# Kernel tuning notes

Measured on AMD Instinct MI355X. Metric: run time of the kernel, lower is better.

## Reference

```python
import jax, jax.numpy as jnp
import numpy as np

H = 64        # hidden_size
G = 64        # global_hidden_size
VOCAB = 128   # VOCAB_SIZE
NUM_OPS = 20
DEPTH = 12    # complete binary tree: 2**DEPTH - 1 nodes
B = 128       # batch of trees
TEMP = 3.0    # self.temperature


def setup_inputs() -> dict:
    key = jax.random.key(0)
    ks = jax.random.split(key, 16)
    s = 0.05
    N = 2 ** DEPTH - 1
    inp = {
        "x_idx": jax.random.randint(ks[0], (B, N), 0, VOCAB, dtype=jnp.int32),
        "validity_mask": jnp.ones((NUM_OPS,), jnp.float32),
        # binary tree-LSTM (blstm): x one-hot -> gates [i, f_a, f_b, o, u]
        "Wx": jax.random.normal(ks[1], (VOCAB, 5 * H), jnp.float32) * s,
        "Ua": jax.random.normal(ks[2], (H, 5 * H), jnp.float32) * s,
        "Ub": jax.random.normal(ks[3], (H, 5 * H), jnp.float32) * s,
        "b_tree": jnp.zeros((5 * H,), jnp.float32),
        # global nn.LSTM (1 layer), gate order i,f,g,o
        "W_ih": jax.random.normal(ks[4], (H, 4 * G), jnp.float32) * s,
        "W_hh": jax.random.normal(ks[5], (G, 4 * G), jnp.float32) * s,
        "b_lstm": jnp.zeros((4 * G,), jnp.float32),
        # FFN on root hidden
        "W1": jax.random.normal(ks[6], (H, H), jnp.float32) * s,
        "b1": jnp.zeros((H,), jnp.float32),
        "W2": jax.random.normal(ks[7], (H, H), jnp.float32) * s,
        "b2": jnp.zeros((H,), jnp.float32),
        # actor head on [hidden ; global_hidden]
        "actor_W": jax.random.normal(ks[8], (H + G, NUM_OPS), jnp.float32) * s,
        "actor_b": jnp.zeros((NUM_OPS,), jnp.float32),
    }
    return inp


def _tree_lstm_sweep(x_idx, Wx, Ua, Ub, b_tree):
    """Bottom-up binary tree-LSTM over a complete binary tree.
    Node i's children sit at flat positions 2i+1, 2i+2 (level layout)."""
    h_prev = c_prev = None
    for d in range(DEPTH - 1, -1, -1):
        n = 2 ** d
        off = n - 1
        # memory-bound gather of gate pre-activations: [B, n, 5H]
        z = Wx[x_idx[:, off:off + n]] + b_tree
        if h_prev is not None:
            h_a, h_b = h_prev[:, 0::2], h_prev[:, 1::2]
            c_a, c_b = c_prev[:, 0::2], c_prev[:, 1::2]
            z = z + jnp.einsum("bnh,hg->bng", h_a, Ua) + jnp.einsum("bnh,hg->bng", h_b, Ub)
        i, fa, fb, o, u = jnp.split(z, 5, axis=-1)
        c = jax.nn.sigmoid(i) * jnp.tanh(u)
        if h_prev is not None:
            c = c + jax.nn.sigmoid(fa) * c_a + jax.nn.sigmoid(fb) * c_b
        h = jax.nn.sigmoid(o) * jnp.tanh(c)
        h_prev, c_prev = h, c
    return h_prev[:, 0]  # root hidden [B, H]


def reference(x_idx, validity_mask, Wx, Ua, Ub, b_tree, W_ih, W_hh, b_lstm,
              W1, b1, W2, b2, actor_W, actor_b):
    h_root = _tree_lstm_sweep(x_idx, Wx, Ua, Ub, b_tree)
    # internal op 1: apply_ffn then apply_global_lstm
    f = jnp.maximum(h_root @ W1 + b1, 0.0) @ W2 + b2          # FFN [B, H]
    h0 = jnp.zeros((f.shape[0], G), f.dtype)
    g = f @ W_ih + h0 @ W_hh + b_lstm                          # one LSTM step
    i, fg, gg, o = jnp.split(g, 4, axis=-1)                    # torch order i,f,g,o
    c_g = jax.nn.sigmoid(i) * jnp.tanh(gg)                     # c0 = 0
    h_g = jax.nn.sigmoid(o) * jnp.tanh(c_g)                    # [B, G]
    # external actor with validity-masked weights (as in policy())
    feats = jnp.concatenate([f, h_g], axis=-1)                 # [B, H+G]
    logits = jnp.log(validity_mask) + feats @ (actor_W * validity_mask) + actor_b * validity_mask
    return jax.nn.softmax(logits / TEMP, axis=-1)              # [B, NUM_OPS]
```

## Files before the change

kernel.cpp:

```cpp
#include <hip/hip_runtime.h>


typedef unsigned short u16;
typedef unsigned int   u32;
typedef __attribute__((ext_vector_type(8))) short  short8;
typedef __attribute__((ext_vector_type(4))) float  floatx4;

#define L2E  1.44269504f
#define L2E2 2.885390082f

__device__ __forceinline__ float frcp(float x) { return __fdividef(1.0f, x); }
__device__ __forceinline__ float fsig(float x) { return frcp(1.0f + __expf(-x)); }
__device__ __forceinline__ float ftanh(float x) {
    return 1.0f - 2.0f * frcp(__expf(2.0f * x) + 1.0f);
}
__device__ __forceinline__ u16 f2bfa(float x) {
    return (u16)((__float_as_uint(x) + 0x8000u) >> 16);
}
__device__ __forceinline__ float bflo(u32 cc) { return __uint_as_float(cc << 16); }
__device__ __forceinline__ float bfhi(u32 cc) { return __uint_as_float(cc & 0xFFFF0000u); }

__device__ __forceinline__ void lstm_gates(
    float zi, float zfa, float zfb, float zo, float zu,
    float ca, float cb, float& c, float& h)
{
    zi  = fmaxf(zi, -60.f);  zfa = fmaxf(zfa, -60.f);
    zfb = fmaxf(zfb, -60.f); zo  = fmaxf(zo, -60.f);
    zu  = fmaxf(zu, -60.f);
    float ei  = __builtin_amdgcn_exp2f(-zi);
    float efa = __builtin_amdgcn_exp2f(-zfa);
    float efb = __builtin_amdgcn_exp2f(-zfb);
    float eo  = __builtin_amdgcn_exp2f(-zo);
    float eu2 = __builtin_amdgcn_exp2f(-zu);
    float pfa = 1.f + efa, pfb = 1.f + efb;
    float cf = (ca * pfb + cb * pfa) * __builtin_amdgcn_rcpf(pfa * pfb);
    c = (1.f - eu2) * __builtin_amdgcn_rcpf((1.f + ei) * (1.f + eu2)) + cf;
    float ec2 = __builtin_amdgcn_exp2f(fminf(-c * L2E2, 80.f));
    h = (1.f - ec2) * __builtin_amdgcn_rcpf((1.f + eo) * (1.f + ec2));
}

#define HS 72

__global__ void precompute_kernel(
    const float* __restrict__ Wx, const float* __restrict__ b_tree,
    const float* __restrict__ Ua, const float* __restrict__ Ub,
    float4* __restrict__ WpA, float* __restrict__ WpU,
    float4* __restrict__ TaA, float2* __restrict__ TaUC,
    float4* __restrict__ TbA, float2* __restrict__ TbUC,
    u16* __restrict__ Uswz)
{
    int v = blockIdx.x;
    int t = threadIdx.x;
    __shared__ float sz[320], sta[320], stb[320], sh[64], sc[64];
    float z = Wx[v * 320 + t] + b_tree[t];
    sz[t] = z;
    {
        int f = v * 320 + t;
        int j = f & 7, lane = (f >> 3) & 63, tk = f >> 9;
        int nt = tk % 20, kc = tk / 20;
        int k = kc * 32 + (lane >> 4) * 8 + j;
        int nn = nt * 16 + (lane & 15);
        float uval = (k < 64) ? Ua[k * 320 + nn] : Ub[(k - 64) * 320 + nn];
        uval *= ((nn >> 6) == 4) ? L2E2 : L2E;
        Uswz[f] = (u16)((__float_as_uint(uval) + 0x7FFFu +
                         ((__float_as_uint(uval) >> 16) & 1u)) >> 16);
    }
    __syncthreads();
    if (t < 64) {
        float c = fsig(sz[t]) * ftanh(sz[256 + t]);
        float h = fsig(sz[192 + t]) * ftanh(c);
        sc[t] = c; sh[t] = h;
    }
    __syncthreads();
    float ta = 0.f, tb = 0.f;
    #pragma unroll 8
    for (int k = 0; k < 64; ++k) {
        ta += sh[k] * Ua[k * 320 + t];
        tb += sh[k] * Ub[k * 320 + t];
    }
    sta[t] = ta; stb[t] = tb;
    __syncthreads();
    if (t < 64) {
        int o = (v << 6) + t;
        WpA[o]  = make_float4(sz[t] * L2E, sz[64 + t] * L2E,
                              sz[128 + t] * L2E, sz[192 + t] * L2E);
        WpU[o]  = sz[256 + t] * L2E2;
        TaA[o]  = make_float4(sta[t] * L2E, sta[64 + t] * L2E,
                              sta[128 + t] * L2E, sta[192 + t] * L2E);
        TaUC[o] = make_float2(sta[256 + t] * L2E2, sc[t]);
        TbA[o]  = make_float4(stb[t] * L2E, stb[64 + t] * L2E,
                              stb[128 + t] * L2E, stb[192 + t] * L2E);
        TbUC[o] = make_float2(stb[256 + t] * L2E2, sc[t]);
    }
}

template<int NT, int MODE, int GSRC>
__device__ __forceinline__ void sweep_level(
    const u16* hsrc, const u32* csrc,
    u16* hdst, u16* cdst, u16* hg, u16* cg, float* hroot,
    const short8 Bfrag[4][5],
    const float4* __restrict__ WpA, const float* __restrict__ WpU,
    const int* ids, int lbase, int node0g, int nvalid,
    int lane15, int quad, int wv)
{
    floatx4 acc[NT][5];
    #pragma unroll
    for (int mt = 0; mt < NT; ++mt)
        #pragma unroll
        for (int g = 0; g < 5; ++g) acc[mt][g] = (floatx4){0.f, 0.f, 0.f, 0.f};

    #pragma unroll
    for (int mt = 0; mt < NT; ++mt) {
        #pragma unroll
        for (int kc = 0; kc < 4; ++kc) {
            int child = 2 * (lbase + mt * 16 + lane15) + (kc >> 1);
            const u16* ap = GSRC ? (hsrc + child * 64 + (kc & 1) * 32 + quad * 8)
                                 : (hsrc + child * HS + (kc & 1) * 32 + quad * 8);
            short8 a = *(const short8*)ap;
            #pragma unroll
            for (int g = 0; g < 5; ++g)
                acc[mt][g] = __builtin_amdgcn_mfma_f32_16x16x32_bf16(
                    a, Bfrag[kc][g], acc[mt][g], 0, 0, 0);
        }
    }
    int hh = wv * 16 + lane15;
    #pragma unroll
    for (int mt = 0; mt < NT; ++mt) {
        #pragma unroll
        for (int r = 0; r < 4; ++r) {
            int lrow = lbase + mt * 16 + quad * 4 + r;
            int id = ids[lrow];
            float4 wg = WpA[(id << 6) + hh];
            float  wu = WpU[(id << 6) + hh];
            u32 cc = csrc[lrow * 64 + hh];
            float c, h;
            lstm_gates(acc[mt][0][r] + wg.x, acc[mt][1][r] + wg.y,
                       acc[mt][2][r] + wg.z, acc[mt][3][r] + wg.w,
                       acc[mt][4][r] + wu, bflo(cc), bfhi(cc), c, h);
            if (MODE == 0) {
                hdst[lrow * HS + hh] = f2bfa(h);
                cdst[(lrow >> 1) * 128 + hh * 2 + (lrow & 1)] = f2bfa(c);
            }
            if (MODE == 1) {
                if (lrow < nvalid) {
                    int node = node0g + lrow;
                    hg[node * 64 + hh] = f2bfa(h);
                    cg[(node >> 1) * 128 + hh * 2 + (node & 1)] = f2bfa(c);
                }
            }
            if (MODE == 2) {
                if (lrow == 0) hroot[hh] = h;
            }
        }
    }
}

__device__ __forceinline__ void load_bfrags(short8 Bfrag[4][5],
                                            const u16* __restrict__ Uswz,
                                            int wv, int lane)
{
    #pragma unroll
    for (int kc = 0; kc < 4; ++kc)
        #pragma unroll
        for (int g = 0; g < 5; ++g) {
            int nt = g * 4 + wv;
            Bfrag[kc][g] = *(const short8*)(Uswz + ((kc * 20 + nt) * 64 + lane) * 8);
        }
}

__global__ __launch_bounds__(256, 2) void sweepA_kernel(
    const int* __restrict__ x_idx,
    const float4* __restrict__ WpA, const float* __restrict__ WpU,
    const float4* __restrict__ TaA, const float2* __restrict__ TaUC,
    const float4* __restrict__ TbA, const float2* __restrict__ TbUC,
    const u16* __restrict__ Uswz,
    u16* __restrict__ h3, u16* __restrict__ c3)
{
    __shared__ u16 hA[128 * HS];
    __shared__ u16 cA[64 * 128];
    __shared__ u16 hB[64 * HS];
    __shared__ u16 cB[32 * 128];
    __shared__ int sIds[544];
    int t = threadIdx.x, lane = t & 63, wv = t >> 6;
    int lane15 = lane & 15, quad = lane >> 4;
    int b = blockIdx.x >> 3, st = blockIdx.x & 7;
    const int* xb = x_idx + b * 4095;

    for (int i = t; i < 544; i += 256) {
        int g;
        if      (i < 128) g = 1023 + st * 128 + i;
        else if (i < 384) g = 2047 + st * 256 + (i - 128);
        else if (i < 448) g = 511 + st * 64 + (i - 384);
        else if (i < 480) g = 255 + st * 32 + (i - 448);
        else if (i < 496) g = 127 + st * 16 + (i - 480);
        else if (i < 504) g = 63 + st * 8 + (i - 496);
        else if (i < 508) g = 31 + st * 4 + (i - 504);
        else if (i < 510) g = 15 + st * 2 + (i - 508);
        else if (i == 510) g = 7 + st;
        else g = -1;
        sIds[i] = (g >= 0) ? xb[g] : 0;
    }
    __syncthreads();

    #pragma unroll 4
    for (int rr = 0; rr < 32; ++rr) {
        int rl = wv * 32 + rr;
        int id = sIds[rl], ida = sIds[128 + 2 * rl], idb = sIds[129 + 2 * rl];
        float4 wg = WpA[(id << 6) + lane];   float  wu = WpU[(id << 6) + lane];
        float4 ga = TaA[(ida << 6) + lane];  float2 ua = TaUC[(ida << 6) + lane];
        float4 gb = TbA[(idb << 6) + lane];  float2 ub = TbUC[(idb << 6) + lane];
        float c, h;
        lstm_gates(wg.x + ga.x + gb.x, wg.y + ga.y + gb.y, wg.z + ga.z + gb.z,
                   wg.w + ga.w + gb.w, wu + ua.x + ub.x, ua.y, ub.y, c, h);
        hA[rl * HS + lane] = f2bfa(h);
        cA[(rl >> 1) * 128 + lane * 2 + (rl & 1)] = f2bfa(c);
    }
    short8 Bfrag[4][5];
    load_bfrags(Bfrag, Uswz, wv, lane);
    __syncthreads();
    sweep_level<2, 0, 0>(hA, (const u32*)cA, hB, cB, nullptr, nullptr, nullptr,
                         Bfrag, WpA, WpU, &sIds[384], 0, 0, 64, lane15, quad, wv);
    sweep_level<2, 0, 0>(hA, (const u32*)cA, hB, cB, nullptr, nullptr, nullptr,
                         Bfrag, WpA, WpU, &sIds[384], 32, 0, 64, lane15, quad, wv);
    __syncthreads();
    sweep_level<2, 0, 0>(hB, (const u32*)cB, hA, cA, nullptr, nullptr, nullptr,
                         Bfrag, WpA, WpU, &sIds[448], 0, 0, 32, lane15, quad, wv);
    __syncthreads();
    sweep_level<1, 0, 0>(hA, (const u32*)cA, hB, cB, nullptr, nullptr, nullptr,
                         Bfrag, WpA, WpU, &sIds[480], 0, 0, 16, lane15, quad, wv);
    __syncthreads();
    sweep_level<1, 0, 0>(hB, (const u32*)cB, hA, cA, nullptr, nullptr, nullptr,
                         Bfrag, WpA, WpU, &sIds[496], 0, 0, 8, lane15, quad, wv);
    __syncthreads();
    sweep_level<1, 0, 0>(hA, (const u32*)cA, hB, cB, nullptr, nullptr, nullptr,
                         Bfrag, WpA, WpU, &sIds[504], 0, 0, 4, lane15, quad, wv);
    __syncthreads();
    sweep_level<1, 0, 0>(hB, (const u32*)cB, hA, cA, nullptr, nullptr, nullptr,
                         Bfrag, WpA, WpU, &sIds[508], 0, 0, 2, lane15, quad, wv);
    __syncthreads();
    sweep_level<1, 1, 0>(hA, (const u32*)cA, nullptr, nullptr,
                         h3 + (size_t)b * 512, c3 + (size_t)b * 512, nullptr,
                         Bfrag, WpA, WpU, &sIds[510], 0, st, 1, lane15, quad, wv);
}

__global__ __launch_bounds__(256, 2) void sweepB_kernel(
    const int* __restrict__ x_idx,
    const float4* __restrict__ WpA, const float* __restrict__ WpU,
    const u16* __restrict__ Uswz,
    const u16* __restrict__ h3, const u16* __restrict__ c3,
    const float* __restrict__ W1, const float* __restrict__ b1,
    const float* __restrict__ W2, const float* __restrict__ b2,
    const float* __restrict__ W_ih, const float* __restrict__ b_lstm,
    const float* __restrict__ actor_W, const float* __restrict__ actor_b,
    const float* __restrict__ vm, float* __restrict__ out)
{
    __shared__ u16 hA[32 * HS];
    __shared__ u16 cA[16 * 128];
    __shared__ u16 hB[32 * HS];
    __shared__ u16 cB[16 * 128];
    __shared__ int sIds[32];
    __shared__ float hroot[64];
    int t = threadIdx.x, lane = t & 63, wv = t >> 6;
    int lane15 = lane & 15, quad = lane >> 4;
    int b = blockIdx.x;
    const int* xb = x_idx + b * 4095;
    const u16* h3b = h3 + (size_t)b * 512;
    const u16* c3b = c3 + (size_t)b * 512;

    if (t < 32) sIds[t] = (t < 31) ? xb[t] : 0;
    short8 Bfrag[4][5];
    load_bfrags(Bfrag, Uswz, wv, lane);
    __syncthreads();
    sweep_level<1, 0, 1>(h3b, (const u32*)c3b, hB, cB, nullptr, nullptr, nullptr,
                         Bfrag, WpA, WpU, &sIds[3], 0, 0, 4, lane15, quad, wv);
    __syncthreads();
    sweep_level<1, 0, 0>(hB, (const u32*)cB, hA, cA, nullptr, nullptr, nullptr,
                         Bfrag, WpA, WpU, &sIds[1], 0, 0, 2, lane15, quad, wv);
    __syncthreads();
    sweep_level<1, 2, 0>(hA, (const u32*)cA, nullptr, nullptr, nullptr, nullptr,
                         hroot, Bfrag, WpA, WpU, &sIds[0], 0, 0, 1, lane15, quad, wv);
    __syncthreads();

    if (wv == 0) {
        float a = b1[lane];
        #pragma unroll 8
        for (int k = 0; k < 64; ++k) a += hroot[k] * W1[k * 64 + lane];
        float r1 = fmaxf(a, 0.f);
        float f = b2[lane];
        #pragma unroll 8
        for (int k = 0; k < 64; ++k) f += __shfl(r1, k) * W2[k * 64 + lane];
        float gi = b_lstm[lane], gg = b_lstm[128 + lane], go = b_lstm[192 + lane];
        #pragma unroll 8
        for (int k = 0; k < 64; ++k) {
            float fk = __shfl(f, k);
            gi += fk * W_ih[k * 256 + lane];
            gg += fk * W_ih[k * 256 + 128 + lane];
            go += fk * W_ih[k * 256 + 192 + lane];
        }
        float cg = fsig(gi) * ftanh(gg);
        float hg = fsig(go) * ftanh(cg);
        int tt = (lane < 20) ? lane : 19;
        float dot = 0.f;
        #pragma unroll 8
        for (int k = 0; k < 64; ++k) {
            float fk = __shfl(f, k), hk = __shfl(hg, k);
            dot += fk * actor_W[k * 20 + tt] + hk * actor_W[(64 + k) * 20 + tt];
        }
        float m = vm[tt];
        float lg = logf(m) + dot * m + actor_b[tt] * m;
        float mx = -1e30f;
        #pragma unroll
        for (int j = 0; j < 20; ++j) mx = fmaxf(mx, __shfl(lg, j));
        float s = 0.f;
        #pragma unroll
        for (int j = 0; j < 20; ++j) s += __expf((__shfl(lg, j) - mx) * (1.0f / 3.0f));
        if (lane < 20) out[b * 20 + lane] = __expf((lg - mx) * (1.0f / 3.0f)) / s;
    }
}

extern "C" void kernel_launch(void* const* d_in, const int* in_sizes, int n_in,
                              void* d_out, int out_size, void* d_ws, size_t ws_size,
                              hipStream_t stream)
{
    const int*   x_idx   = (const int*)d_in[0];
    const float* vm      = (const float*)d_in[1];
    const float* Wx      = (const float*)d_in[2];
    const float* Ua      = (const float*)d_in[3];
    const float* Ub      = (const float*)d_in[4];
    const float* b_tree  = (const float*)d_in[5];
    const float* W_ih    = (const float*)d_in[6];
    const float* b_lstm  = (const float*)d_in[8];
    const float* W1      = (const float*)d_in[9];
    const float* b1      = (const float*)d_in[10];
    const float* W2      = (const float*)d_in[11];
    const float* b2      = (const float*)d_in[12];
    const float* actor_W = (const float*)d_in[13];
    const float* actor_b = (const float*)d_in[14];
    float* out = (float*)d_out;

    char* ws = (char*)d_ws;
    float4* WpA  = (float4*)ws;  ws += 128 * 64 * 16;
    float4* TaA  = (float4*)ws;  ws += 128 * 64 * 16;
    float4* TbA  = (float4*)ws;  ws += 128 * 64 * 16;
    float2* TaUC = (float2*)ws;  ws += 128 * 64 * 8;
    float2* TbUC = (float2*)ws;  ws += 128 * 64 * 8;
    float*  WpU  = (float*)ws;   ws += 128 * 64 * 4;
    u16*    h3   = (u16*)ws;     ws += 128 * 512 * 2;
    u16*    c3   = (u16*)ws;     ws += 128 * 512 * 2;
    u16*    Uswz = (u16*)ws;     ws += 128 * 320 * 2;

    precompute_kernel<<<128, 320, 0, stream>>>(Wx, b_tree, Ua, Ub,
                                               WpA, WpU, TaA, TaUC, TbA, TbUC, Uswz);
    sweepA_kernel<<<1024, 256, 0, stream>>>(x_idx, WpA, WpU, TaA, TaUC,
                                            TbA, TbUC, Uswz, h3, c3);
    sweepB_kernel<<<128, 256, 0, stream>>>(x_idx, WpA, WpU, Uswz, h3, c3,
                                           W1, b1, W2, b2, W_ih, b_lstm,
                                           actor_W, actor_b, vm, out);
}
```

Measured before the change: 150.3 us.

## Double sweepA block to 8 waves, splitting node rows across wave pairs

The sweepA kernel now launches 512 threads per block instead of 256. Eight waves split the leaf-pair gather work and the first two MFMA tree levels by row halves, with each half handled by a group of four gate-column waves. The upper levels, which have few rows, still run on the first four waves while the rest idle at the barriers. The aim is more latency hiding and a shorter critical path per block. The cost is higher register pressure under launch_bounds(512,2), every wave holding its own B fragments, and idle waves during the later levels.

```diff
diff --git a/kernel.cpp b/kernel.cpp
--- a/kernel.cpp
+++ b/kernel.cpp
@@ -101,7 +101,7 @@
     const short8 Bfrag[4][5],
     const float4* __restrict__ WpA, const float* __restrict__ WpU,
     const int* ids, int lbase, int node0g, int nvalid,
-    int lane15, int quad, int wv)
+    int lane15, int quad, int wg)
 {
     floatx4 acc[NT][5];
     #pragma unroll
@@ -123,19 +123,19 @@
                     a, Bfrag[kc][g], acc[mt][g], 0, 0, 0);
         }
     }
-    int hh = wv * 16 + lane15;
+    int hh = wg * 16 + lane15;
     #pragma unroll
     for (int mt = 0; mt < NT; ++mt) {
         #pragma unroll
         for (int r = 0; r < 4; ++r) {
             int lrow = lbase + mt * 16 + quad * 4 + r;
             int id = ids[lrow];
-            float4 wg = WpA[(id << 6) + hh];
-            float  wu = WpU[(id << 6) + hh];
+            float4 wgv = WpA[(id << 6) + hh];
+            float  wu  = WpU[(id << 6) + hh];
             u32 cc = csrc[lrow * 64 + hh];
             float c, h;
-            lstm_gates(acc[mt][0][r] + wg.x, acc[mt][1][r] + wg.y,
-                       acc[mt][2][r] + wg.z, acc[mt][3][r] + wg.w,
+            lstm_gates(acc[mt][0][r] + wgv.x, acc[mt][1][r] + wgv.y,
+                       acc[mt][2][r] + wgv.z, acc[mt][3][r] + wgv.w,
                        acc[mt][4][r] + wu, bflo(cc), bfhi(cc), c, h);
             if (MODE == 0) {
                 hdst[lrow * HS + hh] = f2bfa(h);
@@ -157,18 +157,18 @@
 
 __device__ __forceinline__ void load_bfrags(short8 Bfrag[4][5],
                                             const u16* __restrict__ Uswz,
-                                            int wv, int lane)
+                                            int wg, int lane)
 {
     #pragma unroll
     for (int kc = 0; kc < 4; ++kc)
         #pragma unroll
         for (int g = 0; g < 5; ++g) {
-            int nt = g * 4 + wv;
+            int nt = g * 4 + wg;
             Bfrag[kc][g] = *(const short8*)(Uswz + ((kc * 20 + nt) * 64 + lane) * 8);
         }
 }
 
-__global__ __launch_bounds__(256, 2) void sweepA_kernel(
+__global__ __launch_bounds__(512, 2) void sweepA_kernel(
     const int* __restrict__ x_idx,
     const float4* __restrict__ WpA, const float* __restrict__ WpU,
     const float4* __restrict__ TaA, const float2* __restrict__ TaUC,
@@ -182,11 +182,12 @@
     __shared__ u16 cB[32 * 128];
     __shared__ int sIds[544];
     int t = threadIdx.x, lane = t & 63, wv = t >> 6;
+    int wg = wv & 3, wm = wv >> 2;
     int lane15 = lane & 15, quad = lane >> 4;
     int b = blockIdx.x >> 3, st = blockIdx.x & 7;
     const int* xb = x_idx + b * 4095;
 
-    for (int i = t; i < 544; i += 256) {
+    for (int i = t; i < 544; i += 512) {
         int g;
         if      (i < 128) g = 1023 + st * 128 + i;
         else if (i < 384) g = 2047 + st * 256 + (i - 128);
@@ -203,44 +204,47 @@
     __syncthreads();
 
     #pragma unroll 4
-    for (int rr = 0; rr < 32; ++rr) {
-        int rl = wv * 32 + rr;
+    for (int rr = 0; rr < 16; ++rr) {
+        int rl = wv * 16 + rr;
         int id = sIds[rl], ida = sIds[128 + 2 * rl], idb = sIds[129 + 2 * rl];
-        float4 wg = WpA[(id << 6) + lane];   float  wu = WpU[(id << 6) + lane];
+        float4 wgv = WpA[(id << 6) + lane];  float  wu = WpU[(id << 6) + lane];
         float4 ga = TaA[(ida << 6) + lane];  float2 ua = TaUC[(ida << 6) + lane];
         float4 gb = TbA[(idb << 6) + lane];  float2 ub = TbUC[(idb << 6) + lane];
         float c, h;
-        lstm_gates(wg.x + ga.x + gb.x, wg.y + ga.y + gb.y, wg.z + ga.z + gb.z,
-                   wg.w + ga.w + gb.w, wu + ua.x + ub.x, ua.y, ub.y, c, h);
+        lstm_gates(wgv.x + ga.x + gb.x, wgv.y + ga.y + gb.y, wgv.z + ga.z + gb.z,
+                   wgv.w + ga.w + gb.w, wu + ua.x + ub.x, ua.y, ub.y, c, h);
         hA[rl * HS + lane] = f2bfa(h);
         cA[(rl >> 1) * 128 + lane * 2 + (rl & 1)] = f2bfa(c);
     }
     short8 Bfrag[4][5];
-    load_bfrags(Bfrag, Uswz, wv, lane);
+    load_bfrags(Bfrag, Uswz, wg, lane);
     __syncthreads();
     sweep_level<2, 0, 0>(hA, (const u32*)cA, hB, cB, nullptr, nullptr, nullptr,
-                         Bfrag, WpA, WpU, &sIds[384], 0, 0, 64, lane15, quad, wv);
-    sweep_level<2, 0, 0>(hA, (const u32*)cA, hB, cB, nullptr, nullptr, nullptr,
-                         Bfrag, WpA, WpU, &sIds[384], 32, 0, 64, lane15, quad, wv);
-    __syncthreads();
-    sweep_level<2, 0, 0>(hB, (const u32*)cB, hA, cA, nullptr, nullptr, nullptr,
-                         Bfrag, WpA, WpU, &sIds[448], 0, 0, 32, lane15, quad, wv);
-    __syncthreads();
-    sweep_level<1, 0, 0>(hA, (const u32*)cA, hB, cB, nullptr, nullptr, nullptr,
-                         Bfrag, WpA, WpU, &sIds[480], 0, 0, 16, lane15, quad, wv);
+                         Bfrag, WpA, WpU, &sIds[384], wm * 32, 0, 64, lane15, quad, wg);
     __syncthreads();
     sweep_level<1, 0, 0>(hB, (const u32*)cB, hA, cA, nullptr, nullptr, nullptr,
-                         Bfrag, WpA, WpU, &sIds[496], 0, 0, 8, lane15, quad, wv);
-    __syncthreads();
-    sweep_level<1, 0, 0>(hA, (const u32*)cA, hB, cB, nullptr, nullptr, nullptr,
-                         Bfrag, WpA, WpU, &sIds[504], 0, 0, 4, lane15, quad, wv);
-    __syncthreads();
-    sweep_level<1, 0, 0>(hB, (const u32*)cB, hA, cA, nullptr, nullptr, nullptr,
-                         Bfrag, WpA, WpU, &sIds[508], 0, 0, 2, lane15, quad, wv);
-    __syncthreads();
-    sweep_level<1, 1, 0>(hA, (const u32*)cA, nullptr, nullptr,
-                         h3 + (size_t)b * 512, c3 + (size_t)b * 512, nullptr,
-                         Bfrag, WpA, WpU, &sIds[510], 0, st, 1, lane15, quad, wv);
+                         Bfrag, WpA, WpU, &sIds[448], wm * 16, 0, 32, lane15, quad, wg);
+    __syncthreads();
+    if (wm == 0)
+        sweep_level<1, 0, 0>(hA, (const u32*)cA, hB, cB, nullptr, nullptr, nullptr,
+                             Bfrag, WpA, WpU, &sIds[480], 0, 0, 16, lane15, quad, wg);
+    __syncthreads();
+    if (wm == 0)
+        sweep_level<1, 0, 0>(hB, (const u32*)cB, hA, cA, nullptr, nullptr, nullptr,
+                             Bfrag, WpA, WpU, &sIds[496], 0, 0, 8, lane15, quad, wg);
+    __syncthreads();
+    if (wm == 0)
+        sweep_level<1, 0, 0>(hA, (const u32*)cA, hB, cB, nullptr, nullptr, nullptr,
+                             Bfrag, WpA, WpU, &sIds[504], 0, 0, 4, lane15, quad, wg);
+    __syncthreads();
+    if (wm == 0)
+        sweep_level<1, 0, 0>(hB, (const u32*)cB, hA, cA, nullptr, nullptr, nullptr,
+                             Bfrag, WpA, WpU, &sIds[508], 0, 0, 2, lane15, quad, wg);
+    __syncthreads();
+    if (wm == 0)
+        sweep_level<1, 1, 0>(hA, (const u32*)cA, nullptr, nullptr,
+                             h3 + (size_t)b * 512, c3 + (size_t)b * 512, nullptr,
+                             Bfrag, WpA, WpU, &sIds[510], 0, st, 1, lane15, quad, wg);
 }
 
 __global__ __launch_bounds__(256, 2) void sweepB_kernel(
@@ -351,7 +355,7 @@
 
     precompute_kernel<<<128, 320, 0, stream>>>(Wx, b_tree, Ua, Ub,
                                                WpA, WpU, TaA, TaUC, TbA, TbUC, Uswz);
-    sweepA_kernel<<<1024, 256, 0, stream>>>(x_idx, WpA, WpU, TaA, TaUC,
+    sweepA_kernel<<<1024, 512, 0, stream>>>(x_idx, WpA, WpU, TaA, TaUC,
                                             TbA, TbUC, Uswz, h3, c3);
     sweepB_kernel<<<128, 256, 0, stream>>>(x_idx, WpA, WpU, Uswz, h3, c3,
                                            W1, b1, W2, b2, W_ih, b_lstm,
```

New measurement: 158.7 us. +5.6%, slower.
